# Kernel optimization log

Measured on AMD Instinct MI355X. Metric: run time of the kernel, lower is better.

Reference implementation:

```python
import jax, jax.numpy as jnp
import numpy as np

IN_F = 4096      # in_features (d_model)
OUT_F = 16384    # out_features (4*d_model FFN)
N_TOK = 8192     # tokens = batch*seq
K = OUT_F // 2   # number of kept output rows (static for jit)


def setup_inputs() -> dict:
    key = jax.random.key(0)
    k1, k2, k3, k4 = jax.random.split(key, 4)
    data = jax.random.normal(k1, (N_TOK, IN_F), jnp.float32)
    weight = jax.random.normal(k2, (OUT_F, IN_F), jnp.float32) * 0.02
    bias = jax.random.normal(k3, (OUT_F,), jnp.float32) * 0.02
    # mask with exactly K ones at random positions (static count -> jit-safe)
    perm = jax.random.permutation(k4, OUT_F)
    mask = jnp.zeros((OUT_F,), jnp.int32).at[perm[:K]].set(1)
    return {"data": data, "weight": weight, "bias": bias, "mask": mask}


def reference(data, weight, bias, mask):
    # mask.nonzero()[0] -> selected output-feature indices (ascending, as torch)
    idx = jnp.nonzero(mask, size=K)[0]                 # [K]
    w_sel = jnp.take(weight, idx, axis=0)              # [K, IN_F] row gather
    b_sel = jnp.take(bias, idx, axis=0)                # [K]
    # F.linear: data @ w_sel^T + b_sel  -> [N_TOK, K]
    return jnp.einsum('ti,ki->tk', data, w_sel) + b_sel
```

## Files before the change

kernel.cpp:

```cpp
#include <hip/hip_runtime.h>
#include <hip/hip_bf16.h>

typedef __bf16 bf16_t;
typedef __attribute__((ext_vector_type(8))) __bf16 bf16x8;
typedef __attribute__((ext_vector_type(4))) float f32x4;

constexpr int IN_F  = 4096;
constexpr int OUT_F = 16384;
constexpr int N_TOK = 8192;
constexpr int KSEL  = 8192;
constexpr long A_ELEMS = (long)N_TOK * IN_F;

constexpr int BM = 256, BN = 256, BK = 64;
constexpr int NT = IN_F / BK;
constexpr int HALF_E = 128 * BK;

#define GLOBAL_CAST(p) (const __attribute__((address_space(1))) void*)(p)
#define LDS_CAST(p)    (__attribute__((address_space(3))) void*)(p)

__global__ __launch_bounds__(1024) void build_idx_kernel(
    const int* __restrict__ mask, const float* __restrict__ bias,
    int* __restrict__ idx, float* __restrict__ bsel)
{
    const int t    = threadIdx.x;
    const int lane = t & 63;
    const int wave = t >> 6;
    const int base_i = t * 16;

    int m[16];
    const int4* mp = (const int4*)(mask + base_i);
#pragma unroll
    for (int v = 0; v < 4; ++v) {
        int4 q = mp[v];
        m[v*4+0] = q.x; m[v*4+1] = q.y; m[v*4+2] = q.z; m[v*4+3] = q.w;
    }
    int cnt = 0;
#pragma unroll
    for (int j = 0; j < 16; ++j) cnt += (m[j] != 0) ? 1 : 0;

    int incl = cnt;
#pragma unroll
    for (int d = 1; d < 64; d <<= 1) {
        int o = __shfl_up(incl, (unsigned)d);
        if (lane >= d) incl += o;
    }

    __shared__ int wsum[16];
    __shared__ int wbase[16];
    if (lane == 63) wsum[wave] = incl;
    __syncthreads();
    if (t == 0) {
        int s = 0;
        for (int w = 0; w < 16; ++w) { wbase[w] = s; s += wsum[w]; }
    }
    __syncthreads();

    int p = wbase[wave] + (incl - cnt);
#pragma unroll
    for (int j = 0; j < 16; ++j) {
        if (m[j]) {
            int i = base_i + j;
            idx[p]  = i;
            bsel[p] = bias[i];
            ++p;
        }
    }
}

__global__ __launch_bounds__(256) void convert_kernel(
    const float* __restrict__ A, const float* __restrict__ W,
    const int* __restrict__ idx,
    bf16_t* __restrict__ Ab, bf16_t* __restrict__ Wb)
{
    const long nvecA = A_ELEMS / 8;
    const long total = nvecA * 2;
    const long stride = (long)gridDim.x * blockDim.x;
    for (long v = (long)blockIdx.x * blockDim.x + threadIdx.x; v < total; v += stride) {
        const float4* src;
        bf16_t* dst;
        if (v < nvecA) {
            src = (const float4*)(A + v * 8);
            dst = Ab + v * 8;
        } else {
            long u = v - nvecA;
            int j = (int)(u >> 9);
            int k = (int)(u & 511) * 8;
            src = (const float4*)(W + (long)idx[j] * IN_F + k);
            dst = Wb + u * 8;
        }
        float4 x = src[0], y = src[1];
        bf16x8 o;
        o[0]=(bf16_t)x.x; o[1]=(bf16_t)x.y; o[2]=(bf16_t)x.z; o[3]=(bf16_t)x.w;
        o[4]=(bf16_t)y.x; o[5]=(bf16_t)y.y; o[6]=(bf16_t)y.z; o[7]=(bf16_t)y.w;
        *(bf16x8*)dst = o;
    }
}

__global__ __launch_bounds__(512, 2) void gemm8p_kernel(
    const bf16_t* __restrict__ A, const bf16_t* __restrict__ B,
    const float* __restrict__ bsel, float* __restrict__ C)
{
    __shared__ __attribute__((aligned(16))) bf16_t As[2][2][HALF_E];
    __shared__ __attribute__((aligned(16))) bf16_t Bs[2][2][HALF_E];

    const int tid  = threadIdx.x;
    const int w    = tid >> 6;
    const int lane = tid & 63;
    const int wr   = w >> 2;
    const int wc   = w & 3;

    const int bid = blockIdx.x;
    const int swz = (bid & 7) * 128 + (bid >> 3);
    const int m0 = (swz & 31) * BM;
    const int n0 = (swz >> 5) * BN;

    const int pr  = lane >> 3;
    const int csw = ((lane & 7) ^ pr) * 8;
    const bf16_t* aSrc[2][2];
    const bf16_t* bSrc[2][2];
#pragma unroll
    for (int h = 0; h < 2; ++h)
#pragma unroll
        for (int j = 0; j < 2; ++j) {
            const int row = h * 128 + (w * 2 + j) * 8 + pr;
            aSrc[h][j] = A + (long)(m0 + row) * IN_F + csw;
            bSrc[h][j] = B + (long)(n0 + row) * IN_F + csw;
        }

#define STAGE_A(buf, h, tl) do {                                               \
    __builtin_amdgcn_global_load_lds(GLOBAL_CAST(aSrc[h][0] + (long)(tl)*BK),  \
        LDS_CAST(&As[buf][h][(w * 2 + 0) * 512]), 16, 0, 0);                   \
    __builtin_amdgcn_global_load_lds(GLOBAL_CAST(aSrc[h][1] + (long)(tl)*BK),  \
        LDS_CAST(&As[buf][h][(w * 2 + 1) * 512]), 16, 0, 0);                   \
} while (0)
#define STAGE_B(buf, h, tl) do {                                               \
    __builtin_amdgcn_global_load_lds(GLOBAL_CAST(bSrc[h][0] + (long)(tl)*BK),  \
        LDS_CAST(&Bs[buf][h][(w * 2 + 0) * 512]), 16, 0, 0);                   \
    __builtin_amdgcn_global_load_lds(GLOBAL_CAST(bSrc[h][1] + (long)(tl)*BK),  \
        LDS_CAST(&Bs[buf][h][(w * 2 + 1) * 512]), 16, 0, 0);                   \
} while (0)

    f32x4 acc[8][4];
#pragma unroll
    for (int m = 0; m < 8; ++m)
#pragma unroll
        for (int n = 0; n < 4; ++n)
#pragma unroll
            for (int j = 0; j < 4; ++j) acc[m][n][j] = 0.f;

    const int fr    = lane & 15;
    const int kslot = lane >> 4;
    const int sp0 = ((kslot     ^ (fr & 7)) << 3);
    const int sp1 = (((4+kslot) ^ (fr & 7)) << 3);

    bf16x8 af[4][2], bg[4][2];

#define RDA(buf, mq) do {                                                      \
    _Pragma("unroll") for (int mm = 0; mm < 4; ++mm) {                         \
        const int r = ((mq) * 4 + mm) * 16 + fr;                               \
        af[mm][0] = *(const bf16x8*)&As[buf][wr][r * 64 + sp0];                \
        af[mm][1] = *(const bf16x8*)&As[buf][wr][r * 64 + sp1];                \
    } } while (0)
#define RDB(buf, nh) do {                                                      \
    _Pragma("unroll") for (int nn = 0; nn < 2; ++nn) {                         \
        const int r = (wc & 1) * 64 + ((nh) * 2 + nn) * 16 + fr;               \
        bg[(nh)*2+nn][0] = *(const bf16x8*)&Bs[buf][wc >> 1][r * 64 + sp0];    \
        bg[(nh)*2+nn][1] = *(const bf16x8*)&Bs[buf][wc >> 1][r * 64 + sp1];    \
    } } while (0)
#define MFMAQ(mq, nh) do {                                                     \
    __builtin_amdgcn_s_setprio(1);                                             \
    _Pragma("unroll") for (int mm = 0; mm < 4; ++mm)                           \
    _Pragma("unroll") for (int nn = 0; nn < 2; ++nn) {                         \
        const int m = (mq) * 4 + mm, n = (nh) * 2 + nn;                        \
        acc[m][n] = __builtin_amdgcn_mfma_f32_16x16x32_bf16(                   \
            af[mm][0], bg[n][0], acc[m][n], 0, 0, 0);                          \
        acc[m][n] = __builtin_amdgcn_mfma_f32_16x16x32_bf16(                   \
            af[mm][1], bg[n][1], acc[m][n], 0, 0, 0);                          \
    }                                                                          \
    __builtin_amdgcn_s_setprio(0); } while (0)
#define BAR()    __builtin_amdgcn_s_barrier()
#define LGKM0()  asm volatile("s_waitcnt lgkmcnt(0)" ::: "memory")
#define LGKMH()  asm volatile("s_waitcnt lgkmcnt(8)" ::: "memory")
#define VMC8()   asm volatile("s_waitcnt vmcnt(8)" ::: "memory")
#define VMC0()   asm volatile("s_waitcnt vmcnt(0)" ::: "memory")

    STAGE_A(0, 0, 0); STAGE_A(0, 1, 0); STAGE_B(0, 0, 0); STAGE_B(0, 1, 0);
    STAGE_A(1, 0, 1); STAGE_A(1, 1, 1); STAGE_B(1, 0, 1); STAGE_B(1, 1, 1);
    VMC8(); BAR();

    for (int I = 0; I < NT / 2; ++I) {
        const int t = 2 * I, u = t + 1;
        const bool s2 = (I < NT / 2 - 1);

        RDA(0, 0); RDB(0, 0);
        LGKMH(); BAR(); LGKM0(); MFMAQ(0, 0); BAR();
        RDB(0, 1);
        BAR(); LGKM0(); MFMAQ(0, 1); BAR();
        RDA(0, 1); if (s2) { STAGE_B(0, 0, t + 2); STAGE_B(0, 1, t + 2); }
        BAR(); LGKM0(); MFMAQ(1, 0); BAR();
        if (s2) { STAGE_A(0, 0, t + 2); STAGE_A(0, 1, t + 2); }
        BAR(); MFMAQ(1, 1); if (s2) VMC8(); else VMC0(); BAR();
        RDA(1, 0); RDB(1, 0);
        LGKMH(); BAR(); LGKM0(); MFMAQ(0, 0); BAR();
        RDB(1, 1);
        BAR(); LGKM0(); MFMAQ(0, 1); BAR();
        RDA(1, 1); if (s2) { STAGE_B(1, 0, u + 2); STAGE_B(1, 1, u + 2); }
        BAR(); LGKM0(); MFMAQ(1, 0); BAR();
        if (s2) { STAGE_A(1, 0, u + 2); STAGE_A(1, 1, u + 2); }
        BAR(); MFMAQ(1, 1); if (s2) VMC8(); else VMC0(); BAR();
    }
    VMC0();

#undef STAGE_A
#undef STAGE_B
#undef RDA
#undef RDB
#undef MFMAQ
#undef BAR
#undef LGKM0
#undef LGKMH
#undef VMC8
#undef VMC0

    float b4[4];
#pragma unroll
    for (int n = 0; n < 4; ++n) b4[n] = bsel[n0 + wc * 64 + n * 16 + fr];

    const int rbase = m0 + wr * 128 + kslot * 4;
#pragma unroll
    for (int m = 0; m < 8; ++m)
#pragma unroll
        for (int n = 0; n < 4; ++n) {
            const int col = n0 + wc * 64 + n * 16 + fr;
#pragma unroll
            for (int j = 0; j < 4; ++j)
                C[(long)(rbase + m * 16 + j) * KSEL + col] = acc[m][n][j] + b4[n];
        }
}

__global__ __launch_bounds__(256) void gemm_f32staged_kernel(
    const float* __restrict__ A, const float* __restrict__ W,
    const int* __restrict__ idx, const float* __restrict__ bsel,
    float* __restrict__ C)
{
    constexpr int FBM = 128, FBN = 128, BK2 = 32;
    __shared__ __attribute__((aligned(16))) float Asf[FBM * BK2];
    __shared__ __attribute__((aligned(16))) float Bsf[FBN * BK2];

    const int tid  = threadIdx.x;
    const int wave = tid >> 6;
    const int lane = tid & 63;
    const int wrf  = wave >> 1;
    const int wcf  = wave & 1;

    const int m0 = blockIdx.x * FBM;
    const int n0 = blockIdx.y * FBN;

    const int srow = lane >> 3;
    const int scol = (lane & 7) * 4;

    const float* aptr[4];
    const float* bptr[4];
#pragma unroll
    for (int i = 0; i < 4; ++i) {
        aptr[i] = A + (long)(m0 + wave * 32 + i * 8 + srow) * IN_F + scol;
        const int br = idx[n0 + wave * 32 + i * 8 + srow];
        bptr[i] = W + (long)br * IN_F + scol;
    }

    f32x4 acc[4][4];
#pragma unroll
    for (int m = 0; m < 4; ++m)
#pragma unroll
        for (int n = 0; n < 4; ++n)
#pragma unroll
            for (int j = 0; j < 4; ++j) acc[m][n][j] = 0.f;

    const int fr = lane & 15;
    const int fk = (lane >> 4) * 8;

    for (int k0 = 0; k0 < IN_F; k0 += BK2) {
#pragma unroll
        for (int i = 0; i < 4; ++i) {
            __builtin_amdgcn_global_load_lds(GLOBAL_CAST(aptr[i] + k0),
                LDS_CAST(&Asf[(wave * 32 + i * 8) * BK2]), 16, 0, 0);
            __builtin_amdgcn_global_load_lds(GLOBAL_CAST(bptr[i] + k0),
                LDS_CAST(&Bsf[(wave * 32 + i * 8) * BK2]), 16, 0, 0);
        }
        __syncthreads();

        bf16x8 af[4], bg[4];
#pragma unroll
        for (int m = 0; m < 4; ++m) {
            const float* p = &Asf[(wrf * 64 + m * 16 + fr) * BK2 + fk];
            f32x4 x = *(const f32x4*)p, y = *(const f32x4*)(p + 4);
#pragma unroll
            for (int j = 0; j < 4; ++j) { af[m][j] = (bf16_t)x[j]; af[m][4+j] = (bf16_t)y[j]; }
        }
#pragma unroll
        for (int n = 0; n < 4; ++n) {
            const float* p = &Bsf[(wcf * 64 + n * 16 + fr) * BK2 + fk];
            f32x4 x = *(const f32x4*)p, y = *(const f32x4*)(p + 4);
#pragma unroll
            for (int j = 0; j < 4; ++j) { bg[n][j] = (bf16_t)x[j]; bg[n][4+j] = (bf16_t)y[j]; }
        }
#pragma unroll
        for (int m = 0; m < 4; ++m)
#pragma unroll
            for (int n = 0; n < 4; ++n)
                acc[m][n] = __builtin_amdgcn_mfma_f32_16x16x32_bf16(
                    af[m], bg[n], acc[m][n], 0, 0, 0);
        __syncthreads();
    }

    float b4[4];
#pragma unroll
    for (int n = 0; n < 4; ++n) b4[n] = bsel[n0 + wcf * 64 + n * 16 + fr];

    const int rbase = m0 + wrf * 64 + (lane >> 4) * 4;
#pragma unroll
    for (int m = 0; m < 4; ++m)
#pragma unroll
        for (int n = 0; n < 4; ++n) {
            const int col = n0 + wcf * 64 + n * 16 + fr;
#pragma unroll
            for (int j = 0; j < 4; ++j)
                C[(long)(rbase + m * 16 + j) * KSEL + col] = acc[m][n][j] + b4[n];
        }
}

extern "C" void kernel_launch(void* const* d_in, const int* in_sizes, int n_in,
                              void* d_out, int out_size, void* d_ws, size_t ws_size,
                              hipStream_t stream)
{
    const float* data   = (const float*)d_in[0];
    const float* weight = (const float*)d_in[1];
    const float* bias   = (const float*)d_in[2];
    const int*   mask   = (const int*)d_in[3];
    float*       out    = (float*)d_out;

    char* ws = (char*)d_ws;
    int*   idx  = (int*)ws;
    float* bsel = (float*)(ws + (KSEL * 4));
    bf16_t* Ab  = (bf16_t*)(ws + (KSEL * 8));
    bf16_t* Wb  = Ab + A_ELEMS;

    const size_t NEED = (size_t)KSEL * 8 + (size_t)A_ELEMS * 2 * 2;

    build_idx_kernel<<<1, 1024, 0, stream>>>(mask, bias, idx, bsel);

    if (ws_size >= NEED) {
        convert_kernel<<<2048, 256, 0, stream>>>(data, weight, idx, Ab, Wb);
        gemm8p_kernel<<<1024, 512, 0, stream>>>(Ab, Wb, bsel, out);
    } else {
        dim3 grid(N_TOK / 128, KSEL / 128);
        gemm_f32staged_kernel<<<grid, 256, 0, stream>>>(data, weight, idx, bsel, out);
    }
}
```

Measured before the change: 721.1 us.

## Restructure GEMM main loop into two phases per tile with staggered A/B prefetch

The main loop now reads all four B fragments at once and issues 32 MFMAs per phase, cutting each tile from four barrier-separated quarters to two. The A and B global-to-LDS stages for future tiles are staggered across phases, with A of the next tile staged only one phase ahead, and the waits become vmcnt(4). The aim is fewer barriers and waitcnt stalls and more MFMA work between syncs. In exchange, more fragment registers are live at once, and the shorter prefetch distance for A may expose memory latency.

```diff
diff --git a/kernel.cpp b/kernel.cpp
--- a/kernel.cpp
+++ b/kernel.cpp
@@ -127,17 +127,19 @@
             bSrc[h][j] = B + (long)(n0 + row) * IN_F + csw;
         }
 
-#define STAGE_A(buf, h, tl) do {                                               \
-    __builtin_amdgcn_global_load_lds(GLOBAL_CAST(aSrc[h][0] + (long)(tl)*BK),  \
-        LDS_CAST(&As[buf][h][(w * 2 + 0) * 512]), 16, 0, 0);                   \
-    __builtin_amdgcn_global_load_lds(GLOBAL_CAST(aSrc[h][1] + (long)(tl)*BK),  \
-        LDS_CAST(&As[buf][h][(w * 2 + 1) * 512]), 16, 0, 0);                   \
+#define STAGE_AT(buf, tl) do {                                                 \
+    _Pragma("unroll") for (int h = 0; h < 2; ++h)                              \
+    _Pragma("unroll") for (int j = 0; j < 2; ++j)                              \
+        __builtin_amdgcn_global_load_lds(                                      \
+            GLOBAL_CAST(aSrc[h][j] + (long)(tl) * BK),                         \
+            LDS_CAST(&As[buf][h][(w * 2 + j) * 512]), 16, 0, 0);               \
 } while (0)
-#define STAGE_B(buf, h, tl) do {                                               \
-    __builtin_amdgcn_global_load_lds(GLOBAL_CAST(bSrc[h][0] + (long)(tl)*BK),  \
-        LDS_CAST(&Bs[buf][h][(w * 2 + 0) * 512]), 16, 0, 0);                   \
-    __builtin_amdgcn_global_load_lds(GLOBAL_CAST(bSrc[h][1] + (long)(tl)*BK),  \
-        LDS_CAST(&Bs[buf][h][(w * 2 + 1) * 512]), 16, 0, 0);                   \
+#define STAGE_BT(buf, tl) do {                                                 \
+    _Pragma("unroll") for (int h = 0; h < 2; ++h)                              \
+    _Pragma("unroll") for (int j = 0; j < 2; ++j)                              \
+        __builtin_amdgcn_global_load_lds(                                      \
+            GLOBAL_CAST(bSrc[h][j] + (long)(tl) * BK),                         \
+            LDS_CAST(&Bs[buf][h][(w * 2 + j) * 512]), 16, 0, 0);               \
 } while (0)
 
     f32x4 acc[8][4];
@@ -161,65 +163,65 @@
         af[mm][0] = *(const bf16x8*)&As[buf][wr][r * 64 + sp0];                \
         af[mm][1] = *(const bf16x8*)&As[buf][wr][r * 64 + sp1];                \
     } } while (0)
-#define RDB(buf, nh) do {                                                      \
-    _Pragma("unroll") for (int nn = 0; nn < 2; ++nn) {                         \
-        const int r = (wc & 1) * 64 + ((nh) * 2 + nn) * 16 + fr;               \
-        bg[(nh)*2+nn][0] = *(const bf16x8*)&Bs[buf][wc >> 1][r * 64 + sp0];    \
-        bg[(nh)*2+nn][1] = *(const bf16x8*)&Bs[buf][wc >> 1][r * 64 + sp1];    \
+#define RDB_ALL(buf) do {                                                      \
+    _Pragma("unroll") for (int nn = 0; nn < 4; ++nn) {                         \
+        const int r = (wc & 1) * 64 + nn * 16 + fr;                            \
+        bg[nn][0] = *(const bf16x8*)&Bs[buf][wc >> 1][r * 64 + sp0];           \
+        bg[nn][1] = *(const bf16x8*)&Bs[buf][wc >> 1][r * 64 + sp1];           \
     } } while (0)
-#define MFMAQ(mq, nh) do {                                                     \
+#define MFMAQ2(mq) do {                                                        \
     __builtin_amdgcn_s_setprio(1);                                             \
     _Pragma("unroll") for (int mm = 0; mm < 4; ++mm)                           \
-    _Pragma("unroll") for (int nn = 0; nn < 2; ++nn) {                         \
-        const int m = (mq) * 4 + mm, n = (nh) * 2 + nn;                        \
-        acc[m][n] = __builtin_amdgcn_mfma_f32_16x16x32_bf16(                   \
-            af[mm][0], bg[n][0], acc[m][n], 0, 0, 0);                          \
-        acc[m][n] = __builtin_amdgcn_mfma_f32_16x16x32_bf16(                   \
-            af[mm][1], bg[n][1], acc[m][n], 0, 0, 0);                          \
+    _Pragma("unroll") for (int nn = 0; nn < 4; ++nn) {                         \
+        const int m = (mq) * 4 + mm;                                           \
+        acc[m][nn] = __builtin_amdgcn_mfma_f32_16x16x32_bf16(                  \
+            af[mm][0], bg[nn][0], acc[m][nn], 0, 0, 0);                        \
+        acc[m][nn] = __builtin_amdgcn_mfma_f32_16x16x32_bf16(                  \
+            af[mm][1], bg[nn][1], acc[m][nn], 0, 0, 0);                        \
     }                                                                          \
     __builtin_amdgcn_s_setprio(0); } while (0)
 #define BAR()    __builtin_amdgcn_s_barrier()
 #define LGKM0()  asm volatile("s_waitcnt lgkmcnt(0)" ::: "memory")
-#define LGKMH()  asm volatile("s_waitcnt lgkmcnt(8)" ::: "memory")
-#define VMC8()   asm volatile("s_waitcnt vmcnt(8)" ::: "memory")
+#define VMC4()   asm volatile("s_waitcnt vmcnt(4)" ::: "memory")
 #define VMC0()   asm volatile("s_waitcnt vmcnt(0)" ::: "memory")
 
-    STAGE_A(0, 0, 0); STAGE_A(0, 1, 0); STAGE_B(0, 0, 0); STAGE_B(0, 1, 0);
-    STAGE_A(1, 0, 1); STAGE_A(1, 1, 1); STAGE_B(1, 0, 1); STAGE_B(1, 1, 1);
-    VMC8(); BAR();
+    STAGE_BT(0, 0); STAGE_AT(0, 0); STAGE_BT(1, 1);
+    VMC4(); BAR();
 
     for (int I = 0; I < NT / 2; ++I) {
         const int t = 2 * I, u = t + 1;
         const bool s2 = (I < NT / 2 - 1);
 
-        RDA(0, 0); RDB(0, 0);
-        LGKMH(); BAR(); LGKM0(); MFMAQ(0, 0); BAR();
-        RDB(0, 1);
-        BAR(); LGKM0(); MFMAQ(0, 1); BAR();
-        RDA(0, 1); if (s2) { STAGE_B(0, 0, t + 2); STAGE_B(0, 1, t + 2); }
-        BAR(); LGKM0(); MFMAQ(1, 0); BAR();
-        if (s2) { STAGE_A(0, 0, t + 2); STAGE_A(0, 1, t + 2); }
-        BAR(); MFMAQ(1, 1); if (s2) VMC8(); else VMC0(); BAR();
-        RDA(1, 0); RDB(1, 0);
-        LGKMH(); BAR(); LGKM0(); MFMAQ(0, 0); BAR();
-        RDB(1, 1);
-        BAR(); LGKM0(); MFMAQ(0, 1); BAR();
-        RDA(1, 1); if (s2) { STAGE_B(1, 0, u + 2); STAGE_B(1, 1, u + 2); }
-        BAR(); LGKM0(); MFMAQ(1, 0); BAR();
-        if (s2) { STAGE_A(1, 0, u + 2); STAGE_A(1, 1, u + 2); }
-        BAR(); MFMAQ(1, 1); if (s2) VMC8(); else VMC0(); BAR();
+        RDA(0, 0); RDB_ALL(0);
+        STAGE_AT(1, u);
+        BAR(); LGKM0(); MFMAQ2(0); BAR();
+
+        RDA(0, 1);
+        if (s2) STAGE_BT(0, t + 2);
+        BAR(); LGKM0(); MFMAQ2(1);
+        if (s2) VMC4(); else VMC0();
+        BAR();
+
+        RDA(1, 0); RDB_ALL(1);
+        if (s2) STAGE_AT(0, t + 2);
+        BAR(); LGKM0(); MFMAQ2(0); BAR();
+
+        RDA(1, 1);
+        if (s2) STAGE_BT(1, u + 2);
+        BAR(); LGKM0(); MFMAQ2(1);
+        if (s2) VMC4();
+        BAR();
     }
     VMC0();
 
-#undef STAGE_A
-#undef STAGE_B
+#undef STAGE_AT
+#undef STAGE_BT
 #undef RDA
-#undef RDB
-#undef MFMAQ
+#undef RDB_ALL
+#undef MFMAQ2
 #undef BAR
 #undef LGKM0
-#undef LGKMH
-#undef VMC8
+#undef VMC4
 #undef VMC0
 
     float b4[4];
```

Measured after the change: 723.9 us. No clear change (+0.4%).
